# Performance work log

Hardware: AMD Instinct MI355X
Metric: run time of the kernel (lower is better)

The kernel has to match this reference:

```python
import jax, jax.numpy as jnp
import numpy as np

B, H, T_STEPS = 256, 1024, 128


def setup_inputs() -> dict:
    key = jax.random.key(0)
    ks = jax.random.split(key, 17)
    s = 1.0 / np.sqrt(H)
    def W(k):
        return jax.random.uniform(k, (H, H), jnp.float32, -s, s)
    def b(k):
        return jax.random.uniform(k, (H,), jnp.float32, -s, s)
    names = ["Wif", "Wii", "Wio", "Wic", "Whf", "Whi", "Who", "Whc"]
    d = {}
    for i, n in enumerate(names):
        d[n] = W(ks[i])
        d["b" + n[1:]] = b(ks[8 + i])
    d["x_0"] = jax.random.normal(ks[16], (B, H), jnp.float32)
    d["T"] = T_STEPS
    return d


def reference(Wif, bif, Wii, bii, Wio, bio, Wic, bic,
              Whf, bhf, Whi, bhi, Who, bho, Whc, bhc, x_0, T):
    def step(carry, _):
        x, h, c = carry
        gf = jax.nn.sigmoid(h @ Whf.T + bhf + x @ Wif.T + bif)
        gi = jax.nn.sigmoid(h @ Whi.T + bhi + x @ Wii.T + bii)
        cp = jnp.tanh(h @ Whc.T + bhc + x @ Wic.T + bic)
        c = gf * c + gi * cp
        go = jax.nn.sigmoid(h @ Who.T + bho + x @ Wio.T + bio)
        h = go * jnp.tanh(c)
        return (h, h, c), h  # next x_input is hidden

    h0 = jnp.zeros((B, H), x_0.dtype)
    c0 = jnp.zeros((B, H), x_0.dtype)
    _, hs = jax.lax.scan(step, (x_0, h0, c0), None, length=T - 1)
    # trajectory[0] = x_0, trajectory[t+1] = hidden after step t  -> [T, B, H]
    return jnp.concatenate([x_0[None], hs], axis=0)
```

## Files before the change

### kernel.cpp

```cpp
#include <hip/hip_runtime.h>
#include <stdint.h>


#define BATCH 256
#define HID   1024

typedef __bf16 bf16_t;
typedef bf16_t bf16x8 __attribute__((ext_vector_type(8)));
typedef float  f32x16 __attribute__((ext_vector_type(16)));
typedef float  f32x4  __attribute__((ext_vector_type(4)));
typedef float  f32x2  __attribute__((ext_vector_type(2)));
typedef unsigned int u32;
typedef unsigned long long u64;

#define WC_OFF    (64ull << 20)
#define BIAS_OFF  (72ull << 20)
#define FLAG_OFF  ((72ull << 20) + (1ull << 16))

#define LDS_BYTES 98304

__device__ __forceinline__ void gload_lds16(const void* g, void* l) {
  auto gp = reinterpret_cast<const __attribute__((address_space(1))) unsigned int*>(
      reinterpret_cast<uintptr_t>(g));
  auto lp = reinterpret_cast<__attribute__((address_space(3))) unsigned int*>(
      reinterpret_cast<uintptr_t>(l));
  __builtin_amdgcn_global_load_lds(gp, lp, 16, 0, 0);
}

__global__ __launch_bounds__(256) void k_prep(
    const float* __restrict__ wf, const float* __restrict__ wi_,
    const float* __restrict__ wo, const float* __restrict__ wc,
    const float* __restrict__ hf, const float* __restrict__ hi,
    const float* __restrict__ ho, const float* __restrict__ hc,
    const float* __restrict__ bf_, const float* __restrict__ bi_,
    const float* __restrict__ bo_, const float* __restrict__ bc_,
    const float* __restrict__ hbf, const float* __restrict__ hbi,
    const float* __restrict__ hbo, const float* __restrict__ hbc,
    bf16_t* __restrict__ Wc, bf16_t* __restrict__ Wi, float* __restrict__ bias)
{
  int r = blockIdx.x;
  int j = r >> 2, g = r & 3;
  const float *wip, *whp, *bip, *bhp;
  switch (g) {
    case 0:  wip = wf;  whp = hf; bip = bf_; bhp = hbf; break;
    case 1:  wip = wi_; whp = hi; bip = bi_; bhp = hbi; break;
    case 2:  wip = wo;  whp = ho; bip = bo_; bhp = hbo; break;
    default: wip = wc;  whp = hc; bip = bc_; bhp = hbc; break;
  }
  int k = threadIdx.x * 4;
  f32x4 a = *(const f32x4*)(wip + (size_t)j * HID + k);
  f32x4 b = *(const f32x4*)(whp + (size_t)j * HID + k);
  union { bf16_t h[4]; u64 v; } pc, pi;
#pragma unroll
  for (int t = 0; t < 4; ++t) { pc.h[t] = (bf16_t)(a[t] + b[t]); pi.h[t] = (bf16_t)a[t]; }
  *(u64*)(Wc + (size_t)r * HID + k) = pc.v;
  *(u64*)(Wi + (size_t)r * HID + k) = pi.v;
  if (threadIdx.x == 0) bias[r] = bip[j] + bhp[j];
}

__global__ __launch_bounds__(256) void k_init(
    const float* __restrict__ x0, float* __restrict__ out,
    bf16_t* __restrict__ hsh, u32* __restrict__ flags, int nflags)
{
  int gid = blockIdx.x * 256 + threadIdx.x;
  int i = gid * 4;
  f32x4 v = *(const f32x4*)(x0 + i);
  __builtin_nontemporal_store(v, (f32x4*)(out + i));
  union { bf16_t h[4]; u64 u; } p;
#pragma unroll
  for (int t = 0; t < 4; ++t) p.h[t] = (bf16_t)v[t];
  *(u64*)(hsh + i) = p.u;
  if (gid < nflags) flags[gid] = 0;
}

__global__ __launch_bounds__(512, 2) void k_lstm(
    const bf16_t* __restrict__ Wc, const bf16_t* __restrict__ Wi,
    const float* __restrict__ bias, bf16_t* __restrict__ hsh,
    u32* __restrict__ flags, float* __restrict__ out, int T)
{
  extern __shared__ char lds[];
  float* blds = (float*)(lds + 65536);

  const int tid  = threadIdx.x;
  const int bid  = blockIdx.x;
  const int mt   = bid & 7;
  const int jt   = bid >> 3;
  const int lane = tid & 63;
  const int wv   = tid >> 6;
  const int wn   = wv & 1;
  const int ks   = wv >> 1;
  const int al   = lane & 31, kh = lane >> 5;
  const int row0 = jt << 7;

  if (tid < 128) blds[tid] = bias[row0 + tid];

  const int eb   = tid >> 4;
  const int jp   = (tid & 15) << 1;
  const int bswz = (eb & 7) << 4;
  float cst0 = 0.f, cst1 = 0.f;

  const int aswz = (al & 7) << 4;
  bf16x8 breg0[16], breg1[16];

  for (int s = 1; s < T; ++s) {
    if (s >= 2 && wv == 0) {
      const u32* f = flags + ((size_t)(s - 1) << 8) + (mt << 5);
      u32 v = (lane < 32) ? 0u : 1u;
      if (lane < 32)
        v = __hip_atomic_load(f + lane, __ATOMIC_RELAXED, __HIP_MEMORY_SCOPE_AGENT);
      int guard = 0;
      while (!__all(v != 0) && guard < (1 << 20)) {
        __builtin_amdgcn_s_sleep(1);
        if (lane < 32 && v == 0)
          v = __hip_atomic_load(f + lane, __ATOMIC_RELAXED, __HIP_MEMORY_SCOPE_AGENT);
        ++guard;
      }
    }
    __syncthreads();

    {
      const char* hp = (const char*)hsh + ((size_t)(s - 1) << 19) + ((size_t)mt << 16);
#pragma unroll
      for (int c = 0; c < 8; ++c) {
        int d = (c << 13) + (tid << 4);
        int row = d >> 11, off = d & 2047;
        gload_lds16(hp + row * 2048 + (off ^ ((row & 7) << 4)), lds + d);
      }
    }
    if (s <= 2) {
      const bf16_t* WB  = (s == 1) ? Wi : Wc;
      const bf16_t* wb0 = WB + ((size_t)(row0 + (wn << 6) + al) << 10) + (ks << 8) + (kh << 3);
      const bf16_t* wb1 = wb0 + (32 << 10);
#pragma unroll
      for (int kk = 0; kk < 16; ++kk) {
        breg0[kk] = *(const bf16x8*)(wb0 + (kk << 4));
        breg1[kk] = *(const bf16x8*)(wb1 + (kk << 4));
      }
    }
    asm volatile("s_waitcnt vmcnt(0)" ::: "memory");
    __syncthreads();

    f32x16 acc0 = {}, acc1 = {};
    {
      const char* abase = lds + al * 2048;
      const int kb0 = (ks << 9) + (kh << 4);
#pragma unroll
      for (int kk = 0; kk < 16; ++kk) {
        bf16x8 a = *(const bf16x8*)(abase + ((kb0 + (kk << 5)) ^ aswz));
        acc0 = __builtin_amdgcn_mfma_f32_32x32x16_bf16(a, breg0[kk], acc0, 0, 0, 0);
        acc1 = __builtin_amdgcn_mfma_f32_32x32x16_bf16(a, breg1[kk], acc1, 0, 0, 0);
      }
    }
    __syncthreads();

#pragma unroll
    for (int r = 0; r < 16; ++r) {
      int prow = (r & 3) + ((r >> 2) << 3) + (kh << 2);
      char* pb = lds + (ks << 14) + prow * 512;
      int sw = (prow & 7) << 4;
      *(float*)(pb + ((((wn << 6) + al) << 2) ^ sw))      = acc0[r];
      *(float*)(pb + ((((wn << 6) + 32 + al) << 2) ^ sw)) = acc1[r];
    }
    __syncthreads();

    float hv[2];
#pragma unroll
    for (int e = 0; e < 2; ++e) {
      int cb = (jp + e) << 4;
      int co = cb ^ bswz;
      const char* pb = lds + eb * 512;
      f32x4 p = *(const f32x4*)(pb + co);
      p += *(const f32x4*)(pb + 16384 + co);
      p += *(const f32x4*)(pb + 32768 + co);
      p += *(const f32x4*)(pb + 49152 + co);
      f32x4 bb = *(const f32x4*)((const char*)blds + cb);
      float xf = p[0] + bb[0], xi = p[1] + bb[1], xo = p[2] + bb[2], xc = p[3] + bb[3];
      float gf = 1.f / (1.f + __expf(-xf));
      float gi = 1.f / (1.f + __expf(-xi));
      float go = 1.f / (1.f + __expf(-xo));
      float cp = tanhf(xc);
      float &cs = e ? cst1 : cst0;
      cs = gf * cs + gi * cp;
      hv[e] = go * tanhf(cs);
    }
    union { bf16_t h2[2]; u32 u; } pk;
    pk.h2[0] = (bf16_t)hv[0]; pk.h2[1] = (bf16_t)hv[1];
    size_t eoff = ((size_t)s << 18) + ((size_t)((mt << 5) + eb) << 10) + (jt << 5) + jp;
    __hip_atomic_store((u32*)(hsh + eoff), pk.u, __ATOMIC_RELAXED, __HIP_MEMORY_SCOPE_AGENT);
    f32x2 ov; ov[0] = hv[0]; ov[1] = hv[1];
    __builtin_nontemporal_store(ov, (f32x2*)(out + eoff));

    asm volatile("s_waitcnt vmcnt(0)" ::: "memory");
    __syncthreads();
    if (tid == 0)
      __hip_atomic_store(flags + ((size_t)s << 8) + (mt << 5) + jt, 1u,
                         __ATOMIC_RELAXED, __HIP_MEMORY_SCOPE_AGENT);
  }
}

extern "C" void kernel_launch(void* const* d_in, const int* in_sizes, int n_in,
                              void* d_out, int out_size, void* d_ws, size_t ws_size,
                              hipStream_t stream) {
  const float* Wif = (const float*)d_in[0];
  const float* bif = (const float*)d_in[1];
  const float* Wii = (const float*)d_in[2];
  const float* bii = (const float*)d_in[3];
  const float* Wio = (const float*)d_in[4];
  const float* bio = (const float*)d_in[5];
  const float* Wic = (const float*)d_in[6];
  const float* bic = (const float*)d_in[7];
  const float* Whf = (const float*)d_in[8];
  const float* bhf = (const float*)d_in[9];
  const float* Whi = (const float*)d_in[10];
  const float* bhi = (const float*)d_in[11];
  const float* Who = (const float*)d_in[12];
  const float* bho = (const float*)d_in[13];
  const float* Whc = (const float*)d_in[14];
  const float* bhc = (const float*)d_in[15];
  const float* x0  = (const float*)d_in[16];
  const int T = out_size / (BATCH * HID);

  char* ws = (char*)d_ws;
  bf16_t* hsh  = (bf16_t*)ws;
  bf16_t* WcP  = (bf16_t*)(ws + WC_OFF);
  bf16_t* WiP  = hsh + ((size_t)(T - 16) << 18);
  float*  bias = (float*)(ws + BIAS_OFF);
  u32*    flg  = (u32*)(ws + FLAG_OFF);
  float*  out  = (float*)d_out;

  hipFuncSetAttribute((const void*)k_lstm,
                      hipFuncAttributeMaxDynamicSharedMemorySize, LDS_BYTES);

  k_prep<<<4096, 256, 0, stream>>>(Wif, Wii, Wio, Wic, Whf, Whi, Who, Whc,
                                   bif, bii, bio, bic, bhf, bhi, bho, bhc,
                                   WcP, WiP, bias);
  k_init<<<256, 256, 0, stream>>>(x0, out, hsh, flg, T * 256);
  k_lstm<<<256, 512, LDS_BYTES, stream>>>(WcP, WiP, bias, hsh, flg, out, T);
}
```

Measured before the change: 736.7 us.

## Replace block barrier flag publish with per-wave counter flags and drop barriers

Each of the 8 waves now publishes its slice of the new hidden state with its own atomic increment on the step flag. Consumers spin until the counter reaches 8, which removes the end-of-step block barrier. Partial sums move to a separate LDS region, so the barrier between the MFMA loop and the partial-sum writes can go; LDS per block grows to about 128 KB. The two setup kernels are merged into one launch, and the h-tile swizzle widens from 8 to 16 rows to reduce bank conflicts. In exchange there are 8 atomics per flag instead of one store, and the larger LDS footprint limits residency to one block per CU.

```diff
diff --git a/kernel.cpp b/kernel.cpp
--- a/kernel.cpp
+++ b/kernel.cpp
@@ -17,7 +17,7 @@
 #define BIAS_OFF  (72ull << 20)
 #define FLAG_OFF  ((72ull << 20) + (1ull << 16))
 
-#define LDS_BYTES 98304
+#define LDS_BYTES 131584
 
 __device__ __forceinline__ void gload_lds16(const void* g, void* l) {
   auto gp = reinterpret_cast<const __attribute__((address_space(1))) unsigned int*>(
@@ -27,7 +27,7 @@
   __builtin_amdgcn_global_load_lds(gp, lp, 16, 0, 0);
 }
 
-__global__ __launch_bounds__(256) void k_prep(
+__global__ __launch_bounds__(256) void k_setup(
     const float* __restrict__ wf, const float* __restrict__ wi_,
     const float* __restrict__ wo, const float* __restrict__ wc,
     const float* __restrict__ hf, const float* __restrict__ hi,
@@ -36,41 +36,40 @@
     const float* __restrict__ bo_, const float* __restrict__ bc_,
     const float* __restrict__ hbf, const float* __restrict__ hbi,
     const float* __restrict__ hbo, const float* __restrict__ hbc,
-    bf16_t* __restrict__ Wc, bf16_t* __restrict__ Wi, float* __restrict__ bias)
-{
-  int r = blockIdx.x;
-  int j = r >> 2, g = r & 3;
-  const float *wip, *whp, *bip, *bhp;
-  switch (g) {
-    case 0:  wip = wf;  whp = hf; bip = bf_; bhp = hbf; break;
-    case 1:  wip = wi_; whp = hi; bip = bi_; bhp = hbi; break;
-    case 2:  wip = wo;  whp = ho; bip = bo_; bhp = hbo; break;
-    default: wip = wc;  whp = hc; bip = bc_; bhp = hbc; break;
-  }
-  int k = threadIdx.x * 4;
-  f32x4 a = *(const f32x4*)(wip + (size_t)j * HID + k);
-  f32x4 b = *(const f32x4*)(whp + (size_t)j * HID + k);
-  union { bf16_t h[4]; u64 v; } pc, pi;
-#pragma unroll
-  for (int t = 0; t < 4; ++t) { pc.h[t] = (bf16_t)(a[t] + b[t]); pi.h[t] = (bf16_t)a[t]; }
-  *(u64*)(Wc + (size_t)r * HID + k) = pc.v;
-  *(u64*)(Wi + (size_t)r * HID + k) = pi.v;
-  if (threadIdx.x == 0) bias[r] = bip[j] + bhp[j];
-}
-
-__global__ __launch_bounds__(256) void k_init(
     const float* __restrict__ x0, float* __restrict__ out,
+    bf16_t* __restrict__ Wc, bf16_t* __restrict__ Wi, float* __restrict__ bias,
     bf16_t* __restrict__ hsh, u32* __restrict__ flags, int nflags)
 {
-  int gid = blockIdx.x * 256 + threadIdx.x;
-  int i = gid * 4;
-  f32x4 v = *(const f32x4*)(x0 + i);
-  __builtin_nontemporal_store(v, (f32x4*)(out + i));
-  union { bf16_t h[4]; u64 u; } p;
-#pragma unroll
-  for (int t = 0; t < 4; ++t) p.h[t] = (bf16_t)v[t];
-  *(u64*)(hsh + i) = p.u;
-  if (gid < nflags) flags[gid] = 0;
+  int bid = blockIdx.x;
+  if (bid < 4096) {
+    int r = bid, j = r >> 2, g = r & 3;
+    const float *wip, *whp, *bip, *bhp;
+    switch (g) {
+      case 0:  wip = wf;  whp = hf; bip = bf_; bhp = hbf; break;
+      case 1:  wip = wi_; whp = hi; bip = bi_; bhp = hbi; break;
+      case 2:  wip = wo;  whp = ho; bip = bo_; bhp = hbo; break;
+      default: wip = wc;  whp = hc; bip = bc_; bhp = hbc; break;
+    }
+    int k = threadIdx.x * 4;
+    f32x4 a = *(const f32x4*)(wip + (size_t)j * HID + k);
+    f32x4 b = *(const f32x4*)(whp + (size_t)j * HID + k);
+    union { bf16_t h[4]; u64 v; } pc, pi;
+#pragma unroll
+    for (int t = 0; t < 4; ++t) { pc.h[t] = (bf16_t)(a[t] + b[t]); pi.h[t] = (bf16_t)a[t]; }
+    *(u64*)(Wc + (size_t)r * HID + k) = pc.v;
+    *(u64*)(Wi + (size_t)r * HID + k) = pi.v;
+    if (threadIdx.x == 0) bias[r] = bip[j] + bhp[j];
+  } else {
+    int gid = (bid - 4096) * 256 + threadIdx.x;
+    int i = gid * 4;
+    f32x4 v = *(const f32x4*)(x0 + i);
+    __builtin_nontemporal_store(v, (f32x4*)(out + i));
+    union { bf16_t h[4]; u64 u; } p;
+#pragma unroll
+    for (int t = 0; t < 4; ++t) p.h[t] = (bf16_t)v[t];
+    *(u64*)(hsh + i) = p.u;
+    if (gid < nflags) flags[gid] = 0;
+  }
 }
 
 __global__ __launch_bounds__(512, 2) void k_lstm(
@@ -79,7 +78,8 @@
     u32* __restrict__ flags, float* __restrict__ out, int T)
 {
   extern __shared__ char lds[];
-  float* blds = (float*)(lds + 65536);
+  char*  plds = lds + 65536;
+  float* blds = (float*)(lds + 131072);
 
   const int tid  = threadIdx.x;
   const int bid  = blockIdx.x;
@@ -97,21 +97,23 @@
   const int eb   = tid >> 4;
   const int jp   = (tid & 15) << 1;
   const int bswz = (eb & 7) << 4;
+  const size_t eoff_base = ((size_t)((mt << 5) + eb) << 10) + (jt << 5) + jp;
   float cst0 = 0.f, cst1 = 0.f;
 
-  const int aswz = (al & 7) << 4;
+  const int aswz = (al & 15) << 4;
+  const int kb0  = (ks << 9) + (kh << 4);
   bf16x8 breg0[16], breg1[16];
 
   for (int s = 1; s < T; ++s) {
     if (s >= 2 && wv == 0) {
       const u32* f = flags + ((size_t)(s - 1) << 8) + (mt << 5);
-      u32 v = (lane < 32) ? 0u : 1u;
-      if (lane < 32)
-        v = __hip_atomic_load(f + lane, __ATOMIC_RELAXED, __HIP_MEMORY_SCOPE_AGENT);
+      u32 v = (lane < 32)
+          ? __hip_atomic_load(f + lane, __ATOMIC_RELAXED, __HIP_MEMORY_SCOPE_AGENT)
+          : 8u;
       int guard = 0;
-      while (!__all(v != 0) && guard < (1 << 20)) {
+      while (__any(v != 8u) && guard < (1 << 20)) {
         __builtin_amdgcn_s_sleep(1);
-        if (lane < 32 && v == 0)
+        if (lane < 32 && v != 8u)
           v = __hip_atomic_load(f + lane, __ATOMIC_RELAXED, __HIP_MEMORY_SCOPE_AGENT);
         ++guard;
       }
@@ -124,7 +126,7 @@
       for (int c = 0; c < 8; ++c) {
         int d = (c << 13) + (tid << 4);
         int row = d >> 11, off = d & 2047;
-        gload_lds16(hp + row * 2048 + (off ^ ((row & 7) << 4)), lds + d);
+        gload_lds16(hp + row * 2048 + (off ^ ((row & 15) << 4)), lds + d);
       }
     }
     if (s <= 2) {
@@ -143,7 +145,6 @@
     f32x16 acc0 = {}, acc1 = {};
     {
       const char* abase = lds + al * 2048;
-      const int kb0 = (ks << 9) + (kh << 4);
 #pragma unroll
       for (int kk = 0; kk < 16; ++kk) {
         bf16x8 a = *(const bf16x8*)(abase + ((kb0 + (kk << 5)) ^ aswz));
@@ -151,12 +152,11 @@
         acc1 = __builtin_amdgcn_mfma_f32_32x32x16_bf16(a, breg1[kk], acc1, 0, 0, 0);
       }
     }
-    __syncthreads();
 
 #pragma unroll
     for (int r = 0; r < 16; ++r) {
       int prow = (r & 3) + ((r >> 2) << 3) + (kh << 2);
-      char* pb = lds + (ks << 14) + prow * 512;
+      char* pb = plds + (ks << 14) + prow * 512;
       int sw = (prow & 7) << 4;
       *(float*)(pb + ((((wn << 6) + al) << 2) ^ sw))      = acc0[r];
       *(float*)(pb + ((((wn << 6) + 32 + al) << 2) ^ sw)) = acc1[r];
@@ -168,7 +168,7 @@
     for (int e = 0; e < 2; ++e) {
       int cb = (jp + e) << 4;
       int co = cb ^ bswz;
-      const char* pb = lds + eb * 512;
+      const char* pb = plds + eb * 512;
       f32x4 p = *(const f32x4*)(pb + co);
       p += *(const f32x4*)(pb + 16384 + co);
       p += *(const f32x4*)(pb + 32768 + co);
@@ -183,18 +183,18 @@
       cs = gf * cs + gi * cp;
       hv[e] = go * tanhf(cs);
     }
+
     union { bf16_t h2[2]; u32 u; } pk;
     pk.h2[0] = (bf16_t)hv[0]; pk.h2[1] = (bf16_t)hv[1];
-    size_t eoff = ((size_t)s << 18) + ((size_t)((mt << 5) + eb) << 10) + (jt << 5) + jp;
-    __hip_atomic_store((u32*)(hsh + eoff), pk.u, __ATOMIC_RELAXED, __HIP_MEMORY_SCOPE_AGENT);
+    __hip_atomic_store((u32*)(hsh + ((size_t)s << 18) + eoff_base), pk.u,
+                       __ATOMIC_RELAXED, __HIP_MEMORY_SCOPE_AGENT);
+    asm volatile("s_waitcnt vmcnt(0)" ::: "memory");
+    if (lane == 0)
+      __hip_atomic_fetch_add(flags + ((size_t)s << 8) + (mt << 5) + jt, 1u,
+                             __ATOMIC_RELAXED, __HIP_MEMORY_SCOPE_AGENT);
+    asm volatile("" ::: "memory");
     f32x2 ov; ov[0] = hv[0]; ov[1] = hv[1];
-    __builtin_nontemporal_store(ov, (f32x2*)(out + eoff));
-
-    asm volatile("s_waitcnt vmcnt(0)" ::: "memory");
-    __syncthreads();
-    if (tid == 0)
-      __hip_atomic_store(flags + ((size_t)s << 8) + (mt << 5) + jt, 1u,
-                         __ATOMIC_RELAXED, __HIP_MEMORY_SCOPE_AGENT);
+    __builtin_nontemporal_store(ov, (f32x2*)(out + ((size_t)s << 18) + eoff_base));
   }
 }
 
@@ -231,9 +231,8 @@
   hipFuncSetAttribute((const void*)k_lstm,
                       hipFuncAttributeMaxDynamicSharedMemorySize, LDS_BYTES);
 
-  k_prep<<<4096, 256, 0, stream>>>(Wif, Wii, Wio, Wic, Whf, Whi, Who, Whc,
-                                   bif, bii, bio, bic, bhf, bhi, bho, bhc,
-                                   WcP, WiP, bias);
-  k_init<<<256, 256, 0, stream>>>(x0, out, hsh, flg, T * 256);
+  k_setup<<<4352, 256, 0, stream>>>(Wif, Wii, Wio, Wic, Whf, Whi, Who, Whc,
+                                    bif, bii, bio, bic, bhf, bhi, bho, bhc,
+                                    x0, out, WcP, WiP, bias, hsh, flg, T * 256);
   k_lstm<<<256, 512, LDS_BYTES, stream>>>(WcP, WiP, bias, hsh, flg, out, T);
 }
```

Measured after the change: 884.1 us. +20.0%, slower.
